# Kernel optimization log

Hardware: AMD Instinct MI355X
Metric: run time of the kernel (lower is better)

The kernel has to match this reference:

```python
import jax, jax.numpy as jnp
import numpy as np
import math

D_MODEL = 1024
N_HEADS = 16
D_HID = 64
B, L = 2, 2048
NEG = -1e9
EPS = 1e-5


def setup_inputs() -> dict:
    key = jax.random.key(0)
    ks = jax.random.split(key, 16)
    dmh = N_HEADS * D_HID
    s_in = 1.0 / math.sqrt(D_MODEL)
    s_out = 1.0 / math.sqrt(dmh)
    return {
        "Q": jax.random.normal(ks[0], (B, L, D_MODEL), jnp.float32),
        "K": jax.random.normal(ks[1], (B, L, D_MODEL), jnp.float32),
        "V": jax.random.normal(ks[2], (B, L, D_MODEL), jnp.float32),
        "atten_mask": jax.random.randint(ks[3], (B, L, L), 0, 2) > 0,
        "Wq": jax.random.normal(ks[4], (D_MODEL, dmh), jnp.float32) * s_in,
        "bq": jnp.zeros((dmh,), jnp.float32),
        "Wk": jax.random.normal(ks[5], (D_MODEL, dmh), jnp.float32) * s_in,
        "bk": jnp.zeros((dmh,), jnp.float32),
        "Wv": jax.random.normal(ks[6], (D_MODEL, dmh), jnp.float32) * s_in,
        "bv": jnp.zeros((dmh,), jnp.float32),
        "Wo": jax.random.normal(ks[7], (dmh, D_MODEL), jnp.float32) * s_out,
        "bo": jnp.zeros((D_MODEL,), jnp.float32),
        "gamma": jnp.ones((D_MODEL,), jnp.float32),
        "beta": jnp.zeros((D_MODEL,), jnp.float32),
    }


def reference(Q, K, V, atten_mask, Wq, bq, Wk, bk, Wv, bv, Wo, bo, gamma, beta):
    b = Q.shape[0]
    # project and split heads: [B, L, H, Dh] -> [B, H, L, Dh]
    q = (Q @ Wq + bq).reshape(b, -1, N_HEADS, D_HID).transpose(0, 2, 1, 3)
    k = (K @ Wk + bk).reshape(b, -1, N_HEADS, D_HID).transpose(0, 2, 1, 3)
    v = (V @ Wv + bv).reshape(b, -1, N_HEADS, D_HID).transpose(0, 2, 1, 3)
    scale = 1.0 / math.sqrt(D_HID)
    scores = jnp.einsum("bhqd,bhkd->bhqk", q, k * scale)
    scores = jnp.where(atten_mask[:, None, :, :], NEG, scores)
    atten = jax.nn.softmax(scores, axis=-1)
    context = jnp.einsum("bhqk,bhkd->bhqd", atten, v)
    context = context.transpose(0, 2, 1, 3).reshape(b, -1, N_HEADS * D_HID)
    out = context @ Wo + bo
    # residual + LayerNorm
    x = out + Q
    mu = jnp.mean(x, axis=-1, keepdims=True)
    var = jnp.var(x, axis=-1, keepdims=True)
    y = (x - mu) * jax.lax.rsqrt(var + EPS) * gamma + beta
    return (y, atten)
```

## Files before the change

kernel.cpp:

```cpp
#include <hip/hip_runtime.h>
#include <hip/hip_fp16.h>

typedef unsigned short u16;
typedef __attribute__((ext_vector_type(8))) _Float16 f16x8;
typedef __attribute__((ext_vector_type(2))) _Float16 f16x2;
typedef __attribute__((ext_vector_type(4))) float   f32x4;

typedef const __attribute__((address_space(1))) void* gas1_t;
typedef __attribute__((address_space(3))) void*       las3_t;

#define LOG2E 1.44269504089f
#define M12   17.3123404907f

__device__ __forceinline__ void async_ld16(const void* g, void* s){
  __builtin_amdgcn_global_load_lds((gas1_t)g, (las3_t)s, 16, 0, 0);
}
__device__ __forceinline__ u16 f2h(float f){
  return __half_as_ushort(__float2half(f));
}

__global__ void cvt3_kernel(const float* __restrict__ s0, const float* __restrict__ s1,
                            const float* __restrict__ s2, u16* __restrict__ d0,
                            u16* __restrict__ d1, u16* __restrict__ d2)
{
  const float* s = (blockIdx.y==0)? s0 : (blockIdx.y==1)? s1 : s2;
  u16* d = (blockIdx.y==0)? d0 : (blockIdx.y==1)? d1 : d2;
  for(int i = blockIdx.x*256 + threadIdx.x; i < 1048576; i += 512*256){
    float4 v = ((const float4*)s)[i];
    ushort4 o; o.x=f2h(v.x); o.y=f2h(v.y); o.z=f2h(v.z); o.w=f2h(v.w);
    ((ushort4*)d)[i] = o;
  }
}

__global__ void transcvt_kernel(const float* __restrict__ W0, const float* __restrict__ W1,
                                const float* __restrict__ W2, const float* __restrict__ W3,
                                u16* __restrict__ T0, u16* __restrict__ T1,
                                u16* __restrict__ T2, u16* __restrict__ T3)
{
  __shared__ float tile[64][65];
  int z = blockIdx.z;
  const float* W = (z==0)?W0:(z==1)?W1:(z==2)?W2:W3;
  u16* T = (z==0)?T0:(z==1)?T1:(z==2)?T2:T3;
  int k0 = blockIdx.y*64, n0v = blockIdx.x*64;
  int t = threadIdx.x, r = t>>4, c4 = (t&15)*4;
#pragma unroll
  for(int p=0;p<4;p++){
    int rr = p*16 + r;
    float4 v = *(const float4*)&W[(size_t)(k0+rr)*1024 + n0v + c4];
    tile[rr][c4+0]=v.x; tile[rr][c4+1]=v.y; tile[rr][c4+2]=v.z; tile[rr][c4+3]=v.w;
  }
  __syncthreads();
#pragma unroll
  for(int p=0;p<4;p++){
    int rr = p*16 + r;
    ushort4 o;
    o.x = f2h(tile[c4+0][rr]); o.y = f2h(tile[c4+1][rr]);
    o.z = f2h(tile[c4+2][rr]); o.w = f2h(tile[c4+3][rr]);
    *(ushort4*)&T[(size_t)(n0v+rr)*1024 + k0 + c4] = o;
  }
}

__global__ void mask_detect_kernel(const unsigned int* __restrict__ m, int* __restrict__ flag){
  __shared__ int any;
  if(threadIdx.x==0) any = 0;
  __syncthreads();
  int bad = 0;
  for(int i=threadIdx.x;i<2048;i+=256) if(m[i] > 1u) bad = 1;
  if(bad) any = 1;
  __syncthreads();
  if(threadIdx.x==0) *flag = any;
}

__global__ void mask_bits_kernel(const void* __restrict__ msrc, const int* __restrict__ flag,
                                 unsigned long long* __restrict__ mbits)
{
  int gw = (blockIdx.x*256 + threadIdx.x)>>6;
  int lane = threadIdx.x & 63;
  int f = *flag;
  for(int c=0;c<32;c++){
    int idx = gw*2048 + c*64 + lane;
    unsigned v = f ? (unsigned)((const unsigned char*)msrc)[idx]
                   : ((const unsigned int*)msrc)[idx];
    unsigned long long bal = __ballot(v != 0u);
    if(lane==0) mbits[gw*32 + c] = bal;
  }
}

__device__ __forceinline__ void gemm_kloop(const u16* __restrict__ A, const u16* __restrict__ BT,
                                           int m0, int n0, u16* lA, u16* lB, f32x4 acc[4][4])
{
  int t = threadIdx.x, w = t>>6, l = t&63, l4 = l>>4, lm = l&15;
  int wr = w>>1, wc = w&1;
  auto STAGE = [&](int k0, int half){
#pragma unroll
    for(int j=0;j<2;j++){
      int idx = j*4096 + w*1024 + l*16;
      int r = idx>>6, cb = idx&63;
      int cbs = cb ^ ((r&3)<<4);
      async_ld16((const char*)A  + (((size_t)(m0+r))<<11) + k0*2 + cbs,
                 (char*)lA + half*8192 + j*4096 + w*1024);
      async_ld16((const char*)BT + (((size_t)(n0+r))<<11) + k0*2 + cbs,
                 (char*)lB + half*8192 + j*4096 + w*1024);
    }
  };
  STAGE(0, 0);
  __syncthreads();
  for(int kt=0; kt<32; kt++){
    if(kt<31) STAGE((kt+1)*32, (kt+1)&1);
    const char* pA = (const char*)lA + (kt&1)*8192;
    const char* pB = (const char*)lB + (kt&1)*8192;
    f16x8 af[4], bfr[4];
#pragma unroll
    for(int m=0;m<4;m++){
      int ar = wr*64 + m*16 + lm;
      af[m] = *(const f16x8*)(pA + ar*64 + ((l4*16) ^ ((ar&3)<<4)));
    }
#pragma unroll
    for(int n=0;n<4;n++){
      int br = wc*64 + n*16 + lm;
      bfr[n] = *(const f16x8*)(pB + br*64 + ((l4*16) ^ ((br&3)<<4)));
    }
#pragma unroll
    for(int m=0;m<4;m++)
#pragma unroll
      for(int n=0;n<4;n++)
        acc[m][n] = __builtin_amdgcn_mfma_f32_16x16x32_f16(af[m], bfr[n], acc[m][n], 0,0,0);
    __syncthreads();
  }
}

__global__ __launch_bounds__(256) void proj_gemm(
    const u16* __restrict__ Xq, const u16* __restrict__ Xk, const u16* __restrict__ Xv,
    const u16* __restrict__ WqT, const u16* __restrict__ WkT, const u16* __restrict__ WvT,
    const float* __restrict__ bq, const float* __restrict__ bk, const float* __restrict__ bv,
    u16* __restrict__ qb, u16* __restrict__ kbuf, u16* __restrict__ vTb)
{
  __shared__ u16 lA[8192], lB[8192];
  int z = blockIdx.z;
  const u16* A  = (z==0)?Xq :(z==1)?Xk :Xv;
  const u16* BT = (z==0)?WqT:(z==1)?WkT:WvT;
  const float* bias = (z==0)?bq:(z==1)?bk:bv;
  int m0 = blockIdx.y*128, n0 = blockIdx.x*128;
  f32x4 zf = {0.f,0.f,0.f,0.f};
  f32x4 acc[4][4];
#pragma unroll
  for(int m=0;m<4;m++)
#pragma unroll
    for(int n=0;n<4;n++) acc[m][n]=zf;
  gemm_kloop(A, BT, m0, n0, lA, lB, acc);

  int t = threadIdx.x, w = t>>6, l = t&63, l4 = l>>4, lm = l&15;
  int wr = w>>1, wc = w&1;
  float scale = (z==1)? 0.125f : 1.0f;
#pragma unroll
  for(int n=0;n<4;n++){
    int ng = n0 + wc*64 + n*16 + lm;
    float bsv = bias[ng];
#pragma unroll
    for(int m=0;m<4;m++){
      int mb = m0 + wr*64 + m*16 + l4*4;
      f32x4 c = acc[m][n];
      int bhh = ((mb>>11)<<4) + (ng>>6);
      if(z<2){
        u16* dst = (z==0)? qb : kbuf;
        size_t base = (((size_t)bhh)<<17) + ((size_t)(mb&2047)<<6) + (ng&63);
        dst[base      ] = f2h((c[0]+bsv)*scale);
        dst[base +  64] = f2h((c[1]+bsv)*scale);
        dst[base + 128] = f2h((c[2]+bsv)*scale);
        dst[base + 192] = f2h((c[3]+bsv)*scale);
      } else {
        size_t off = (((size_t)bhh)<<17) + ((size_t)(ng&63)<<11) + (mb&2047);
        ushort4 o;
        o.x=f2h(c[0]+bsv); o.y=f2h(c[1]+bsv); o.z=f2h(c[2]+bsv); o.w=f2h(c[3]+bsv);
        *(ushort4*)(vTb + off) = o;
      }
    }
  }
}

__global__ __launch_bounds__(512, 4) void attn_fused(
    const u16* __restrict__ qb, const u16* __restrict__ kb,
    const u16* __restrict__ vTb, const unsigned long long* __restrict__ mbits,
    float* __restrict__ att, u16* __restrict__ ctx)
{
  __shared__ u16 kdb[2][4096];
  __shared__ u16 vdb[2][4096];
  __shared__ u16 pl[8][16*136];
  int bh = blockIdx.y, b = bh>>4, h = bh&15;
  int q0 = blockIdx.x*128;
  int t = threadIdx.x, w = t>>6, l = t&63, l4 = l>>4, lm = l&15;
  int qw = q0 + w*16 + lm;

  const u16* qrow = qb + ((size_t)bh*2048 + qw)*64;
  f16x8 qB0 = *(const f16x8*)(qrow + l4*8);
  f16x8 qB1 = *(const f16x8*)(qrow + 32 + l4*8);

  const unsigned long long* mrow = mbits + (size_t)(b*2048 + qw)*32;
  const char* kbase_b = (const char*)(kb  + ((size_t)bh<<17));
  const char* vbase_b = (const char*)(vTb + ((size_t)bh<<17));
  f32x4 zf = {0.f,0.f,0.f,0.f};

  int srow = t>>3, scb = (t&7)*16;
  auto STAGE_K = [&](int kt, int half){
    async_ld16(kbase_b + (size_t)(kt*64+srow)*128 + (scb ^ ((srow&7)<<4)),
               (char*)kdb[half] + t*16);
  };
  auto STAGE_V = [&](int kt, int half){
    async_ld16(vbase_b + (size_t)srow*4096 + kt*128 + (scb ^ ((srow&7)<<4)),
               (char*)vdb[half] + t*16);
  };

  float esum = 0.f;
  STAGE_K(0,0);
  __syncthreads();
  for(int kt=0;kt<32;kt++){
    if(kt<31) STAGE_K(kt+1, (kt+1)&1);
    const char* kbuf_h = (const char*)kdb[kt&1];
    unsigned long long mw = mrow[kt];
    unsigned mlo = (unsigned)mw, mhi = (unsigned)(mw>>32);
    __builtin_amdgcn_s_setprio(1);
#pragma unroll
    for(int kf=0;kf<4;kf++){
      int keyr = kf*16 + lm, sw = (keyr&7)<<4;
      const char* kp = kbuf_h + keyr*128;
      f16x8 a0 = *(const f16x8*)(kp + ((l4*16) ^ sw));
      f16x8 a1 = *(const f16x8*)(kp + ((64 + l4*16) ^ sw));
      f32x4 s = __builtin_amdgcn_mfma_f32_16x16x32_f16(a0, qB0, zf, 0,0,0);
      s = __builtin_amdgcn_mfma_f32_16x16x32_f16(a1, qB1, s, 0,0,0);
      unsigned nib = (((kf&2)?mhi:mlo) >> ((kf&1)*16 + l4*4)) & 15u;
      esum += exp2f(((nib&1u)? -1e9f : s[0])*LOG2E - M12);
      esum += exp2f(((nib&2u)? -1e9f : s[1])*LOG2E - M12);
      esum += exp2f(((nib&4u)? -1e9f : s[2])*LOG2E - M12);
      esum += exp2f(((nib&8u)? -1e9f : s[3])*LOG2E - M12);
    }
    __builtin_amdgcn_s_setprio(0);
    __syncthreads();
  }
  esum += __shfl_xor(esum, 16);
  esum += __shfl_xor(esum, 32);
  float lrs = -M12 - log2f(fmaxf(esum, 1e-30f));

  f32x4 cacc[4] = {zf,zf,zf,zf};
  int q_hi = l>>5, koff = (l&31)*4;
  float* abase = att + ((size_t)bh*2048 + q0 + w*16)*2048;
  u16* plw = &pl[w][0];

  STAGE_K(0,0); STAGE_V(0,0);
  __syncthreads();
  for(int kg=0; kg<16; kg++){
#pragma unroll
    for(int km=0; km<2; km++){
      int kt = kg*2 + km;
      if(kt<31){ STAGE_K(kt+1,(kt+1)&1); STAGE_V(kt+1,(kt+1)&1); }
      const char* kbuf_h = (const char*)kdb[kt&1];
      const char* vbuf_h = (const char*)vdb[kt&1];
      unsigned long long mw = mrow[kt];
      unsigned mlo = (unsigned)mw, mhi = (unsigned)(mw>>32);
      __builtin_amdgcn_s_setprio(1);
#pragma unroll
      for(int kf=0;kf<4;kf++){
        int keyr = kf*16 + lm, sw = (keyr&7)<<4;
        const char* kp = kbuf_h + keyr*128;
        f16x8 a0 = *(const f16x8*)(kp + ((l4*16) ^ sw));
        f16x8 a1 = *(const f16x8*)(kp + ((64 + l4*16) ^ sw));
        f32x4 s = __builtin_amdgcn_mfma_f32_16x16x32_f16(a0, qB0, zf, 0,0,0);
        s = __builtin_amdgcn_mfma_f32_16x16x32_f16(a1, qB1, s, 0,0,0);
        unsigned nib = (((kf&2)?mhi:mlo) >> ((kf&1)*16 + l4*4)) & 15u;
        float p0 = exp2f(((nib&1u)? -1e9f : s[0])*LOG2E + lrs);
        float p1 = exp2f(((nib&2u)? -1e9f : s[1])*LOG2E + lrs);
        float p2 = exp2f(((nib&4u)? -1e9f : s[2])*LOG2E + lrs);
        float p3 = exp2f(((nib&8u)? -1e9f : s[3])*LOG2E + lrs);
        uint2 pk;
        pk.x = __builtin_bit_cast(unsigned, __builtin_amdgcn_cvt_pkrtz(p0,p1));
        pk.y = __builtin_bit_cast(unsigned, __builtin_amdgcn_cvt_pkrtz(p2,p3));
        *(uint2*)(plw + lm*136 + km*64 + kf*16 + l4*4) = pk;
      }
#pragma unroll
      for(int kk=0;kk<2;kk++){
        f16x8 pb = *(const f16x8*)(plw + lm*136 + km*64 + kk*32 + l4*8);
#pragma unroll
        for(int mf=0;mf<4;mf++){
          int dr = mf*16 + lm;
          const char* vp = vbuf_h + dr*128;
          f16x8 av = *(const f16x8*)(vp + ((kk*64 + l4*16) ^ ((dr&7)<<4)));
          cacc[mf] = __builtin_amdgcn_mfma_f32_16x16x32_f16(av, pb, cacc[mf], 0,0,0);
        }
      }
      __builtin_amdgcn_s_setprio(0);
      __syncthreads();
    }
#pragma unroll
    for(int qq=0; qq<16; qq+=2){
      int q = qq + q_hi;
      uint2 ph = *(const uint2*)(plw + q*136 + koff);
      f16x2 h0 = __builtin_bit_cast(f16x2, ph.x);
      f16x2 h1 = __builtin_bit_cast(f16x2, ph.y);
      f32x4 o4 = { (float)h0[0], (float)h0[1], (float)h1[0], (float)h1[1] };
      __builtin_nontemporal_store(o4,
          (f32x4*)(abase + (size_t)q*2048 + kg*128 + koff));
    }
  }
  int token = b*2048 + qw;
#pragma unroll
  for(int mf=0;mf<4;mf++){
    ushort4 o;
    o.x=f2h(cacc[mf][0]); o.y=f2h(cacc[mf][1]);
    o.z=f2h(cacc[mf][2]); o.w=f2h(cacc[mf][3]);
    *(ushort4*)(ctx + (size_t)token*1024 + h*64 + mf*16 + l4*4) = o;
  }
}

__global__ __launch_bounds__(256) void out_gemm(
    const u16* __restrict__ ctx, const u16* __restrict__ WoT,
    const float* __restrict__ bo, const float* __restrict__ Qres, float* __restrict__ xout)
{
  __shared__ u16 lA[8192], lB[8192];
  int m0 = blockIdx.y*128, n0 = blockIdx.x*128;
  f32x4 zf = {0.f,0.f,0.f,0.f};
  f32x4 acc[4][4];
#pragma unroll
  for(int m=0;m<4;m++)
#pragma unroll
    for(int n=0;n<4;n++) acc[m][n]=zf;
  gemm_kloop(ctx, WoT, m0, n0, lA, lB, acc);

  int t = threadIdx.x, w = t>>6, l = t&63, l4 = l>>4, lm = l&15;
  int wr = w>>1, wc = w&1;
#pragma unroll
  for(int n=0;n<4;n++){
    int ng = n0 + wc*64 + n*16 + lm;
    float bsv = bo[ng];
#pragma unroll
    for(int m=0;m<4;m++){
      int mb = m0 + wr*64 + m*16 + l4*4;
      f32x4 c = acc[m][n];
#pragma unroll
      for(int j=0;j<4;j++){
        size_t o = ((size_t)(mb+j)<<10) + ng;
        xout[o] = c[j] + bsv + Qres[o];
      }
    }
  }
}

__global__ void ln_kernel(const float* __restrict__ x, const float* __restrict__ gamma,
                          const float* __restrict__ beta, float* __restrict__ y)
{
  int row = blockIdx.x, t = threadIdx.x;
  float4 v = ((const float4*)(x + (size_t)row*1024))[t];
  float s  = v.x+v.y+v.z+v.w;
  float sq = v.x*v.x + v.y*v.y + v.z*v.z + v.w*v.w;
#pragma unroll
  for(int d=1; d<64; d<<=1){ s += __shfl_xor(s, d); sq += __shfl_xor(sq, d); }
  __shared__ float red[8];
  int w = t>>6, l = t&63;
  if(l==0){ red[w] = s; red[4+w] = sq; }
  __syncthreads();
  s  = red[0]+red[1]+red[2]+red[3];
  sq = red[4]+red[5]+red[6]+red[7];
  float mu  = s * 0.0009765625f;
  float var = sq * 0.0009765625f - mu*mu;
  float rs  = rsqrtf(var + 1e-5f);
  float4 g  = ((const float4*)gamma)[t];
  float4 be = ((const float4*)beta)[t];
  float4 o;
  o.x = (v.x-mu)*rs*g.x + be.x;
  o.y = (v.y-mu)*rs*g.y + be.y;
  o.z = (v.z-mu)*rs*g.z + be.z;
  o.w = (v.w-mu)*rs*g.w + be.w;
  ((float4*)(y + (size_t)row*1024))[t] = o;
}

extern "C" void kernel_launch(void* const* d_in, const int* in_sizes, int n_in,
                              void* d_out, int out_size, void* d_ws, size_t ws_size,
                              hipStream_t stream)
{
  (void)in_sizes; (void)n_in; (void)out_size; (void)ws_size;
  const float* Q    = (const float*)d_in[0];
  const float* K    = (const float*)d_in[1];
  const float* V    = (const float*)d_in[2];
  const void*  mraw = d_in[3];
  const float* Wq   = (const float*)d_in[4];
  const float* bq   = (const float*)d_in[5];
  const float* Wk   = (const float*)d_in[6];
  const float* bk   = (const float*)d_in[7];
  const float* Wv   = (const float*)d_in[8];
  const float* bv   = (const float*)d_in[9];
  const float* Wo   = (const float*)d_in[10];
  const float* bo   = (const float*)d_in[11];
  const float* gamma= (const float*)d_in[12];
  const float* beta = (const float*)d_in[13];

  char* ws = (char*)d_ws;
  const size_t MB = 1ull<<20;
  u16* WqT  = (u16*)(ws + 0*MB);
  u16* WkT  = (u16*)(ws + 2*MB);
  u16* WvT  = (u16*)(ws + 4*MB);
  u16* WoT  = (u16*)(ws + 6*MB);
  u16* Xq   = (u16*)(ws + 8*MB);
  u16* Xk   = (u16*)(ws + 16*MB);
  u16* Xv   = (u16*)(ws + 24*MB);
  u16* qb   = (u16*)(ws + 32*MB);
  u16* kbuf = (u16*)(ws + 40*MB);
  u16* vTb  = (u16*)(ws + 48*MB);
  u16* ctx  = (u16*)(ws + 56*MB);
  unsigned long long* mbits = (unsigned long long*)(ws + 8*MB);
  int* flag = (int*)(ws + 10*MB);
  float* xres = (float*)(ws + 16*MB);

  float* yout = (float*)d_out;
  float* att  = (float*)d_out + 4194304;

  cvt3_kernel<<<dim3(512,3,1), 256, 0, stream>>>(Q,K,V,Xq,Xk,Xv);
  transcvt_kernel<<<dim3(16,16,4), 256, 0, stream>>>(Wq,Wk,Wv,Wo,WqT,WkT,WvT,WoT);
  proj_gemm<<<dim3(8,32,3), 256, 0, stream>>>(Xq,Xk,Xv,WqT,WkT,WvT,bq,bk,bv,qb,kbuf,vTb);
  mask_detect_kernel<<<1,256,0,stream>>>((const unsigned int*)mraw, flag);
  mask_bits_kernel<<<1024,256,0,stream>>>(mraw, flag, mbits);
  attn_fused<<<dim3(16,32), 512, 0, stream>>>(qb,kbuf,vTb,mbits,att,ctx);
  out_gemm<<<dim3(8,32), 256, 0, stream>>>(ctx,WoT,bo,Q,xres);
  ln_kernel<<<4096, 256, 0, stream>>>(xres,gamma,beta,yout);
}
```

Baseline: 277.7 us.

## Deepen K prefetch in stats pass and shrink P staging for higher occupancy

The first softmax-statistics pass now prefetches K two tiles ahead, reusing the idle V buffers as a four-slot ring, and replaces the full __syncthreads with a partial vmcnt wait plus s_barrier. The second pass drops the two-tile grouping: the per-warp P staging buffer is cut from 136 to 72 halves per row, and attention probabilities are written out every 64-key tile. Launch bounds are raised from 4 to 6 blocks per CU, which the smaller LDS footprint makes possible. The hand-written vmcnt counts depend on the exact number and order of outstanding memory operations, so a wrong count could cause stale reads, and the higher occupancy target may force register spills.

```diff
diff --git a/kernel.cpp b/kernel.cpp
--- a/kernel.cpp
+++ b/kernel.cpp
@@ -178,14 +178,14 @@
   }
 }
 
-__global__ __launch_bounds__(512, 4) void attn_fused(
+__global__ __launch_bounds__(512, 6) void attn_fused(
     const u16* __restrict__ qb, const u16* __restrict__ kb,
     const u16* __restrict__ vTb, const unsigned long long* __restrict__ mbits,
     float* __restrict__ att, u16* __restrict__ ctx)
 {
   __shared__ u16 kdb[2][4096];
   __shared__ u16 vdb[2][4096];
-  __shared__ u16 pl[8][16*136];
+  __shared__ u16 pl[8][1152];
   int bh = blockIdx.y, b = bh>>4, h = bh&15;
   int q0 = blockIdx.x*128;
   int t = threadIdx.x, w = t>>6, l = t&63, l4 = l>>4, lm = l&15;
@@ -201,9 +201,9 @@
   f32x4 zf = {0.f,0.f,0.f,0.f};
 
   int srow = t>>3, scb = (t&7)*16;
-  auto STAGE_K = [&](int kt, int half){
-    async_ld16(kbase_b + (size_t)(kt*64+srow)*128 + (scb ^ ((srow&7)<<4)),
-               (char*)kdb[half] + t*16);
+  auto kbuf_at = [&](int kt)->char*{ return (char*)((kt&2)? vdb[kt&1] : kdb[kt&1]); };
+  auto STAGE_K_to = [&](int kt, char* dst){
+    async_ld16(kbase_b + (size_t)(kt*64+srow)*128 + (scb ^ ((srow&7)<<4)), dst + t*16);
   };
   auto STAGE_V = [&](int kt, int half){
     async_ld16(vbase_b + (size_t)srow*4096 + kt*128 + (scb ^ ((srow&7)<<4)),
@@ -211,11 +211,13 @@
   };
 
   float esum = 0.f;
-  STAGE_K(0,0);
+  STAGE_K_to(0, kbuf_at(0));
+  STAGE_K_to(1, kbuf_at(1));
   __syncthreads();
   for(int kt=0;kt<32;kt++){
-    if(kt<31) STAGE_K(kt+1, (kt+1)&1);
-    const char* kbuf_h = (const char*)kdb[kt&1];
+    if(kt<30) STAGE_K_to(kt+2, kbuf_at(kt+2));
+    asm volatile("" ::: "memory");
+    const char* kbuf_h = kbuf_at(kt);
     unsigned long long mw = mrow[kt];
     unsigned mlo = (unsigned)mw, mhi = (unsigned)(mw>>32);
     __builtin_amdgcn_s_setprio(1);
@@ -234,71 +236,74 @@
       esum += exp2f(((nib&8u)? -1e9f : s[3])*LOG2E - M12);
     }
     __builtin_amdgcn_s_setprio(0);
-    __syncthreads();
+    asm volatile("s_waitcnt vmcnt(1)" ::: "memory");
+    __builtin_amdgcn_s_barrier();
+    asm volatile("" ::: "memory");
   }
   esum += __shfl_xor(esum, 16);
   esum += __shfl_xor(esum, 32);
   float lrs = -M12 - log2f(fmaxf(esum, 1e-30f));
 
   f32x4 cacc[4] = {zf,zf,zf,zf};
-  int q_hi = l>>5, koff = (l&31)*4;
+  int qr4 = l>>4, kc4 = (l&15)*4;
   float* abase = att + ((size_t)bh*2048 + q0 + w*16)*2048;
   u16* plw = &pl[w][0];
 
-  STAGE_K(0,0); STAGE_V(0,0);
-  __syncthreads();
-  for(int kg=0; kg<16; kg++){
-#pragma unroll
-    for(int km=0; km<2; km++){
-      int kt = kg*2 + km;
-      if(kt<31){ STAGE_K(kt+1,(kt+1)&1); STAGE_V(kt+1,(kt+1)&1); }
-      const char* kbuf_h = (const char*)kdb[kt&1];
-      const char* vbuf_h = (const char*)vdb[kt&1];
-      unsigned long long mw = mrow[kt];
-      unsigned mlo = (unsigned)mw, mhi = (unsigned)(mw>>32);
-      __builtin_amdgcn_s_setprio(1);
-#pragma unroll
-      for(int kf=0;kf<4;kf++){
-        int keyr = kf*16 + lm, sw = (keyr&7)<<4;
-        const char* kp = kbuf_h + keyr*128;
-        f16x8 a0 = *(const f16x8*)(kp + ((l4*16) ^ sw));
-        f16x8 a1 = *(const f16x8*)(kp + ((64 + l4*16) ^ sw));
-        f32x4 s = __builtin_amdgcn_mfma_f32_16x16x32_f16(a0, qB0, zf, 0,0,0);
-        s = __builtin_amdgcn_mfma_f32_16x16x32_f16(a1, qB1, s, 0,0,0);
-        unsigned nib = (((kf&2)?mhi:mlo) >> ((kf&1)*16 + l4*4)) & 15u;
-        float p0 = exp2f(((nib&1u)? -1e9f : s[0])*LOG2E + lrs);
-        float p1 = exp2f(((nib&2u)? -1e9f : s[1])*LOG2E + lrs);
-        float p2 = exp2f(((nib&4u)? -1e9f : s[2])*LOG2E + lrs);
-        float p3 = exp2f(((nib&8u)? -1e9f : s[3])*LOG2E + lrs);
-        uint2 pk;
-        pk.x = __builtin_bit_cast(unsigned, __builtin_amdgcn_cvt_pkrtz(p0,p1));
-        pk.y = __builtin_bit_cast(unsigned, __builtin_amdgcn_cvt_pkrtz(p2,p3));
-        *(uint2*)(plw + lm*136 + km*64 + kf*16 + l4*4) = pk;
+  __syncthreads();
+  STAGE_K_to(0, (char*)kdb[0]); STAGE_V(0, 0);
+  __syncthreads();
+  for(int kt=0; kt<32; kt++){
+    if(kt<31){ STAGE_K_to(kt+1, (char*)kdb[(kt+1)&1]); STAGE_V(kt+1, (kt+1)&1); }
+    asm volatile("" ::: "memory");
+    const char* kbuf_h = (const char*)kdb[kt&1];
+    const char* vbuf_h = (const char*)vdb[kt&1];
+    unsigned long long mw = mrow[kt];
+    unsigned mlo = (unsigned)mw, mhi = (unsigned)(mw>>32);
+    __builtin_amdgcn_s_setprio(1);
+#pragma unroll
+    for(int kf=0;kf<4;kf++){
+      int keyr = kf*16 + lm, sw = (keyr&7)<<4;
+      const char* kp = kbuf_h + keyr*128;
+      f16x8 a0 = *(const f16x8*)(kp + ((l4*16) ^ sw));
+      f16x8 a1 = *(const f16x8*)(kp + ((64 + l4*16) ^ sw));
+      f32x4 s = __builtin_amdgcn_mfma_f32_16x16x32_f16(a0, qB0, zf, 0,0,0);
+      s = __builtin_amdgcn_mfma_f32_16x16x32_f16(a1, qB1, s, 0,0,0);
+      unsigned nib = (((kf&2)?mhi:mlo) >> ((kf&1)*16 + l4*4)) & 15u;
+      float p0 = exp2f(((nib&1u)? -1e9f : s[0])*LOG2E + lrs);
+      float p1 = exp2f(((nib&2u)? -1e9f : s[1])*LOG2E + lrs);
+      float p2 = exp2f(((nib&4u)? -1e9f : s[2])*LOG2E + lrs);
+      float p3 = exp2f(((nib&8u)? -1e9f : s[3])*LOG2E + lrs);
+      uint2 pk;
+      pk.x = __builtin_bit_cast(unsigned, __builtin_amdgcn_cvt_pkrtz(p0,p1));
+      pk.y = __builtin_bit_cast(unsigned, __builtin_amdgcn_cvt_pkrtz(p2,p3));
+      *(uint2*)(plw + lm*72 + kf*16 + l4*4) = pk;
+    }
+#pragma unroll
+    for(int kk=0;kk<2;kk++){
+      f16x8 pb = *(const f16x8*)(plw + lm*72 + kk*32 + l4*8);
+#pragma unroll
+      for(int mf=0;mf<4;mf++){
+        int dr = mf*16 + lm;
+        const char* vp = vbuf_h + dr*128;
+        f16x8 av = *(const f16x8*)(vp + ((kk*64 + l4*16) ^ ((dr&7)<<4)));
+        cacc[mf] = __builtin_amdgcn_mfma_f32_16x16x32_f16(av, pb, cacc[mf], 0,0,0);
       }
-#pragma unroll
-      for(int kk=0;kk<2;kk++){
-        f16x8 pb = *(const f16x8*)(plw + lm*136 + km*64 + kk*32 + l4*8);
-#pragma unroll
-        for(int mf=0;mf<4;mf++){
-          int dr = mf*16 + lm;
-          const char* vp = vbuf_h + dr*128;
-          f16x8 av = *(const f16x8*)(vp + ((kk*64 + l4*16) ^ ((dr&7)<<4)));
-          cacc[mf] = __builtin_amdgcn_mfma_f32_16x16x32_f16(av, pb, cacc[mf], 0,0,0);
-        }
-      }
-      __builtin_amdgcn_s_setprio(0);
-      __syncthreads();
-    }
-#pragma unroll
-    for(int qq=0; qq<16; qq+=2){
-      int q = qq + q_hi;
-      uint2 ph = *(const uint2*)(plw + q*136 + koff);
+    }
+    __builtin_amdgcn_s_setprio(0);
+    asm volatile("" ::: "memory");
+#pragma unroll
+    for(int ps=0; ps<4; ps++){
+      int q = ps*4 + qr4;
+      uint2 ph = *(const uint2*)(plw + q*72 + kc4);
       f16x2 h0 = __builtin_bit_cast(f16x2, ph.x);
       f16x2 h1 = __builtin_bit_cast(f16x2, ph.y);
       f32x4 o4 = { (float)h0[0], (float)h0[1], (float)h1[0], (float)h1[1] };
       __builtin_nontemporal_store(o4,
-          (f32x4*)(abase + (size_t)q*2048 + kg*128 + koff));
-    }
+          (f32x4*)(abase + (size_t)q*2048 + kt*64 + kc4));
+    }
+    asm volatile("s_waitcnt vmcnt(4)" ::: "memory");
+    __builtin_amdgcn_s_barrier();
+    asm volatile("" ::: "memory");
   }
   int token = b*2048 + qw;
 #pragma unroll
```

Result: slower. 291.7 us (+5.1%).
